# Kernel tuning notes

Measured on AMD Instinct MI355X. Metric: run time of the kernel, lower is better.

The kernel has to match this reference:

```python
import jax, jax.numpy as jnp
import numpy as np

N = 50000      # nodes
E = 800000     # edges (before self loops)
D_IN = 128
HID = 64
HEADS = 8
D_OUT = 10


def setup_inputs() -> dict:
    key = jax.random.key(0)
    ks = jax.random.split(key, 16)
    sc = 0.05
    x = jax.random.normal(ks[0], (N, D_IN), dtype=jnp.float32)
    edge_index = jax.random.randint(ks[1], (2, E), 0, N, dtype=jnp.int64)
    return {
        "x": x,
        "edge_index": edge_index,
        "W1": jax.random.normal(ks[2], (HEADS * HID, D_IN), dtype=jnp.float32) * sc,
        "a1_src": jax.random.normal(ks[3], (HEADS, HID), dtype=jnp.float32) * sc,
        "a1_dst": jax.random.normal(ks[4], (HEADS, HID), dtype=jnp.float32) * sc,
        "b1": jnp.zeros((HEADS * HID,), jnp.float32),
        "W2": jax.random.normal(ks[5], (HID, HEADS * HID), dtype=jnp.float32) * sc,
        "a2_src": jax.random.normal(ks[6], (1, HID), dtype=jnp.float32) * sc,
        "a2_dst": jax.random.normal(ks[7], (1, HID), dtype=jnp.float32) * sc,
        "b2": jnp.zeros((HID,), jnp.float32),
        "W3": jax.random.normal(ks[8], (HID, HID), dtype=jnp.float32) * sc,
        "a3_src": jax.random.normal(ks[9], (1, HID), dtype=jnp.float32) * sc,
        "a3_dst": jax.random.normal(ks[10], (1, HID), dtype=jnp.float32) * sc,
        "b3": jnp.zeros((HID,), jnp.float32),
        "Wc": jax.random.normal(ks[11], (D_OUT, HID), dtype=jnp.float32) * sc,
        "bc": jnp.zeros((D_OUT,), jnp.float32),
    }


def gat_conv(x, src, dst, W, a_src, a_dst, b, concat):
    """PyG GATConv (eval mode, add_self_loops already applied to src/dst)."""
    heads, out_ch = a_src.shape
    n = x.shape[0]
    h = (x @ W.T).reshape(n, heads, out_ch)          # [N, H, C]
    a_s = jnp.einsum('nhc,hc->nh', h, a_src)          # [N, H]
    a_d = jnp.einsum('nhc,hc->nh', h, a_dst)          # [N, H]
    e = jax.nn.leaky_relu(a_s[src] + a_d[dst], 0.2)   # [Etot, H]
    # segment softmax over incoming edges of each destination node
    m = jax.ops.segment_max(e, dst, num_segments=n)
    ex = jnp.exp(e - m[dst])
    s = jax.ops.segment_sum(ex, dst, num_segments=n)
    alpha = ex / (s[dst] + 1e-16)                     # [Etot, H]
    out = jax.ops.segment_sum(h[src] * alpha[:, :, None], dst, num_segments=n)
    if concat:
        out = out.reshape(n, heads * out_ch)
    else:
        out = out.mean(axis=1)
    return out + b


def reference(x, edge_index, W1, a1_src, a1_dst, b1, W2, a2_src, a2_dst, b2,
              W3, a3_src, a3_dst, b3, Wc, bc):
    loops = jnp.arange(N, dtype=edge_index.dtype)
    src = jnp.concatenate([edge_index[0], loops])
    dst = jnp.concatenate([edge_index[1], loops])
    h = jax.nn.elu(gat_conv(x, src, dst, W1, a1_src, a1_dst, b1, True))
    h = jax.nn.elu(gat_conv(h, src, dst, W2, a2_src, a2_dst, b2, False))
    h = jax.nn.elu(gat_conv(h, src, dst, W3, a3_src, a3_dst, b3, False))
    return h @ Wc.T + bc
```

## Files before the change

kernel.cpp:

```cpp
#include <hip/hip_runtime.h>
#include <math.h>

#define N_NODES 50000
#define N_EDGES 800000
#define ETOT    (N_EDGES + N_NODES)
#define COL_CAP (ETOT + 3 * N_NODES + 16)

typedef short bf16x8 __attribute__((ext_vector_type(8)));
typedef float f32x4  __attribute__((ext_vector_type(4)));
typedef float f32x2  __attribute__((ext_vector_type(2)));

__device__ __forceinline__ float b2f(unsigned int u16) {
    return __uint_as_float(u16 << 16);
}
__device__ __forceinline__ unsigned short f2b(float f) {
    unsigned int u = __float_as_uint(f);
    u += 0x7fffu + ((u >> 16) & 1u);
    return (unsigned short)(u >> 16);
}

__global__ __launch_bounds__(256) void k_prep(const float* __restrict__ x,
                                              const float* __restrict__ w1,
                                              const float* __restrict__ w2,
                                              const float* __restrict__ w3,
                                              unsigned short* __restrict__ xb,
                                              unsigned short* __restrict__ o1,
                                              unsigned short* __restrict__ o2,
                                              unsigned short* __restrict__ o3,
                                              int* __restrict__ deg,
                                              int* __restrict__ flag) {
    int i = blockIdx.x * 256 + threadIdx.x;
    if (i < N_NODES) deg[i] = 0;
    if (i == 0) *flag = 0;
    if (i < 512 * 128 / 4) {
        float4 v = ((const float4*)w1)[i];
        ushort2* o = (ushort2*)(o1 + i * 4);
        o[0] = make_ushort2(f2b(v.x), f2b(v.y));
        o[1] = make_ushort2(f2b(v.z), f2b(v.w));
    }
    if (i < 64 * 512 / 4) {
        float4 v = ((const float4*)w2)[i];
        ushort2* o = (ushort2*)(o2 + i * 4);
        o[0] = make_ushort2(f2b(v.x), f2b(v.y));
        o[1] = make_ushort2(f2b(v.z), f2b(v.w));
    }
    if (i < 64 * 64 / 4) {
        float4 v = ((const float4*)w3)[i];
        ushort2* o = (ushort2*)(o3 + i * 4);
        o[0] = make_ushort2(f2b(v.x), f2b(v.y));
        o[1] = make_ushort2(f2b(v.z), f2b(v.w));
    }
    if (i < N_NODES * 128 / 8) {
        const float4* xp = (const float4*)x + (size_t)i * 2;
        float4 v0 = xp[0], v1 = xp[1];
        unsigned int u0 = (unsigned int)f2b(v0.x) | ((unsigned int)f2b(v0.y) << 16);
        unsigned int u1 = (unsigned int)f2b(v0.z) | ((unsigned int)f2b(v0.w) << 16);
        unsigned int u2 = (unsigned int)f2b(v1.x) | ((unsigned int)f2b(v1.y) << 16);
        unsigned int u3 = (unsigned int)f2b(v1.z) | ((unsigned int)f2b(v1.w) << 16);
        *(uint4*)(xb + (size_t)i * 8) = make_uint4(u0, u1, u2, u3);
    }
}

__global__ __launch_bounds__(256) void k_prepu(const float* __restrict__ W1,
                                               const float* __restrict__ a1s,
                                               const float* __restrict__ a1d,
                                               float* __restrict__ U) {
    int h = blockIdx.x;
    int t = threadIdx.x;
    int which = t >> 7, k = t & 127;
    const float* av = which ? a1d : a1s;
    float acc = 0.f;
    for (int c = 0; c < 64; ++c)
        acc += av[h * 64 + c] * W1[(size_t)(h * 64 + c) * 128 + k];
    U[(which * 8 + h) * 128 + k] = acc;
}

__global__ __launch_bounds__(256) void k_attn(const unsigned short* __restrict__ xb,
                                              const float* __restrict__ U,
                                              float* __restrict__ asrc,
                                              float* __restrict__ adst) {
    __shared__ float sU[16 * 132];
    __shared__ unsigned short sX[16 * 136];
    int t = threadIdx.x;
    for (int i = t; i < 2048; i += 256) sU[(i >> 7) * 132 + (i & 127)] = U[i];
    int n0 = blockIdx.x * 16;
    {
        int r = t >> 4, c = (t & 15) * 8;
        *(uint4*)&sX[r * 136 + c] = *(const uint4*)(xb + (size_t)(n0 + r) * 128 + c);
    }
    __syncthreads();
    int nl = t >> 4, o = t & 15;
    const unsigned short* xr = sX + nl * 136;
    const float* ur = sU + o * 132;
    float acc = 0.f;
#pragma unroll 8
    for (int k2 = 0; k2 < 128; ++k2) acc += b2f(xr[k2]) * ur[k2];
    int n = n0 + nl;
    if (o < 8) asrc[n * 8 + o] = acc;
    else       adst[n * 8 + (o - 8)] = acc;
}

__global__ void k_detect(const int* __restrict__ idx, int* __restrict__ flag) {
    int i = blockIdx.x * blockDim.x + threadIdx.x;
    int v = idx[2 * i + 1];
    unsigned long long any = __ballot(v != 0);
    if ((threadIdx.x & 63) == 0 && any) atomicOr(flag, 1);
}

__device__ __forceinline__ int edge_src(const int* idx, int e, int is32) {
    return is32 ? idx[e] : idx[2 * e];
}
__device__ __forceinline__ int edge_dst(const int* idx, int e, int is32) {
    return is32 ? idx[N_EDGES + e] : idx[2 * (N_EDGES + e)];
}

__global__ void k_degree(const int* __restrict__ idx, const int* __restrict__ flag,
                         int* __restrict__ deg) {
    int e = blockIdx.x * blockDim.x + threadIdx.x;
    if (e >= ETOT) return;
    int is32 = *flag;
    int d = (e < N_EDGES) ? edge_dst(idx, e, is32) : (e - N_EDGES);
    atomicAdd(&deg[d], 1);
}

__global__ __launch_bounds__(256) void k_scan1(const int* __restrict__ deg,
                                               int* __restrict__ rowptr,
                                               int* __restrict__ bsum) {
    __shared__ int sd[256];
    int t = threadIdx.x;
    int i = blockIdx.x * 256 + t;
    int v = (i < N_NODES) ? ((deg[i] + 3) & ~3) : 0;
    sd[t] = v;
    __syncthreads();
#pragma unroll
    for (int off = 1; off < 256; off <<= 1) {
        int a = (t >= off) ? sd[t - off] : 0;
        __syncthreads();
        sd[t] += a;
        __syncthreads();
    }
    if (i < N_NODES) rowptr[i] = sd[t] - v;
    if (t == 255) bsum[blockIdx.x] = sd[255];
}

__global__ __launch_bounds__(256) void k_scan2(int* __restrict__ bsum,
                                               int* __restrict__ boff,
                                               int* __restrict__ rowptr,
                                               int nb) {
    __shared__ int sd[256];
    int t = threadIdx.x;
    int v = (t < nb) ? bsum[t] : 0;
    sd[t] = v;
    __syncthreads();
#pragma unroll
    for (int off = 1; off < 256; off <<= 1) {
        int a = (t >= off) ? sd[t - off] : 0;
        __syncthreads();
        sd[t] += a;
        __syncthreads();
    }
    boff[t] = sd[t] - v;
    if (t == 255) rowptr[N_NODES] = sd[255];
}

__global__ __launch_bounds__(256) void k_scan3(int* __restrict__ rowptr,
                                               const int* __restrict__ boff,
                                               const int* __restrict__ deg,
                                               int* __restrict__ cursor,
                                               int* __restrict__ col) {
    int i = blockIdx.x * 256 + threadIdx.x;
    if (i == 0) {
        int tot = rowptr[N_NODES];
        for (int q = 0; q < 16; ++q) col[tot + q] = 0;
    }
    if (i >= N_NODES) return;
    int r = rowptr[i] + boff[blockIdx.x];
    rowptr[i] = r;
    cursor[i] = r;
    int d = deg[i];
    int pd = (d + 3) & ~3;
    for (int p = r + d; p < r + pd; ++p) col[p] = 0;
}

__global__ void k_scatter(const int* __restrict__ idx, const int* __restrict__ flag,
                          int* __restrict__ cursor, int* __restrict__ col) {
    int e = blockIdx.x * blockDim.x + threadIdx.x;
    if (e >= ETOT) return;
    int is32 = *flag;
    int s, d;
    if (e < N_EDGES) { s = edge_src(idx, e, is32); d = edge_dst(idx, e, is32); }
    else             { s = d = e - N_EDGES; }
    int pos = atomicAdd(&cursor[d], 1);
    col[pos] = s;
}

template<int EPI>
__global__ __launch_bounds__(256) void k_gemm(const unsigned short* __restrict__ Ab,
                                              const unsigned short* __restrict__ W,
                                              unsigned short* __restrict__ C,
                                              const float* __restrict__ a_src,
                                              const float* __restrict__ a_dst,
                                              float* __restrict__ asb,
                                              float* __restrict__ adb,
                                              const float* __restrict__ bias,
                                              int M, int K, int Astr, int aoffmul,
                                              int Nout, int Hstr) {
    __shared__ unsigned short As[64 * 40];
    __shared__ unsigned short Bs[64 * 40];
    __shared__ float red_s[4][64];
    __shared__ float red_d[4][64];
    int t = threadIdx.x;
    int w = t >> 6, l = t & 63;
    int quad = l >> 4, lm = l & 15;
    int m0 = blockIdx.y * 64, n0 = blockIdx.x * 64;
    int hd = blockIdx.x;
    int aoff = hd * aoffmul;
    int lr = t >> 2;
    int lc = (t & 3) * 8;

    f32x4 acc[4];
#pragma unroll
    for (int r = 0; r < 4; ++r) acc[r] = (f32x4){0.f, 0.f, 0.f, 0.f};

    for (int k0 = 0; k0 < K; k0 += 32) {
        int m = m0 + lr;
        uint4 av = make_uint4(0, 0, 0, 0);
        if (m < M) av = *(const uint4*)(Ab + (size_t)m * Astr + aoff + k0 + lc);
        *(uint4*)&As[lr * 40 + lc] = av;
        uint4 bv = *(const uint4*)(W + (size_t)(n0 + lr) * K + k0 + lc);
        *(uint4*)&Bs[lr * 40 + lc] = bv;
        __syncthreads();

        bf16x8 bfrag = *(const bf16x8*)&Bs[(w * 16 + lm) * 40 + quad * 8];
#pragma unroll
        for (int r = 0; r < 4; ++r) {
            bf16x8 afrag = *(const bf16x8*)&As[(r * 16 + lm) * 40 + quad * 8];
            acc[r] = __builtin_amdgcn_mfma_f32_16x16x32_bf16(afrag, bfrag, acc[r], 0, 0, 0);
        }
        __syncthreads();
    }

    if (EPI == 1) {
        float bcol = bias[n0 + w * 16 + lm];
#pragma unroll
        for (int r = 0; r < 4; ++r)
#pragma unroll
            for (int g = 0; g < 4; ++g) {
                int m = m0 + r * 16 + quad * 4 + g;
                if (m < M) {
                    float v = acc[r][g] + bcol;
                    v = (v > 0.f) ? v : expm1f(v);
                    C[(size_t)m * Nout + n0 + w * 16 + lm] = f2b(v);
                }
            }
        return;
    }

#pragma unroll
    for (int r = 0; r < 4; ++r)
#pragma unroll
        for (int g = 0; g < 4; ++g) {
            int m = m0 + r * 16 + quad * 4 + g;
            if (m < M) C[(size_t)m * Nout + n0 + w * 16 + lm] = f2b(acc[r][g]);
        }

    float as = a_src[hd * 64 + w * 16 + lm];
    float ad = a_dst[hd * 64 + w * 16 + lm];
#pragma unroll
    for (int r = 0; r < 4; ++r) {
#pragma unroll
        for (int g = 0; g < 4; ++g) {
            float vs = acc[r][g] * as;
            float vd = acc[r][g] * ad;
#pragma unroll
            for (int off = 1; off < 16; off <<= 1) {
                vs += __shfl_xor(vs, off);
                vd += __shfl_xor(vd, off);
            }
            if (lm == 0) {
                red_s[w][r * 16 + quad * 4 + g] = vs;
                red_d[w][r * 16 + quad * 4 + g] = vd;
            }
        }
    }
    __syncthreads();
    if (t < 64) {
        float vs = red_s[0][t] + red_s[1][t] + red_s[2][t] + red_s[3][t];
        float vd = red_d[0][t] + red_d[1][t] + red_d[2][t] + red_d[3][t];
        int m = m0 + t;
        if (m < M) {
            asb[(size_t)m * Hstr + hd] = vs;
            adb[(size_t)m * Hstr + hd] = vd;
        }
    }
}

__device__ __forceinline__ void aggx_slot(int idx, int rem, float tt, unsigned int xx,
                                          float adn, float& ssum, f32x2* acc) {
    float e = tt + adn;
    e = fmaxf(e, 0.2f * e);
    float ex = __expf(e);
    ex = (idx < rem) ? ex : 0.f;
    ssum += ex;
    float fx = __uint_as_float(xx << 16);
    float fy = __uint_as_float(xx & 0xffff0000u);
    int exi = __float_as_int(ex);
#pragma unroll
    for (int hh = 0; hh < 8; ++hh) {
        float wh = __int_as_float(__builtin_amdgcn_readlane(exi, hh << 3));
        acc[hh].x = fmaf(fx, wh, acc[hh].x);
        acc[hh].y = fmaf(fy, wh, acc[hh].y);
    }
}

__global__ __launch_bounds__(256) void k_aggx(const unsigned short* __restrict__ xb,
                                              const float* __restrict__ asrc,
                                              const float* __restrict__ adst,
                                              const int* __restrict__ rowptr,
                                              const int* __restrict__ degv,
                                              const int* __restrict__ col,
                                              unsigned short* __restrict__ aggX) {
    int n = blockIdx.x * 4 + (threadIdx.x >> 6);
    if (n >= N_NODES) return;
    int l = threadIdx.x & 63;
    int j = l >> 3;
    unsigned lx2 = (unsigned)(l << 1);
    int start = rowptr[n];
    int end   = start + degv[n];
    float adn = adst[((unsigned)n << 3) + (unsigned)j];

    float ssum = 0.f;
    f32x2 acc[8];
#pragma unroll
    for (int hh = 0; hh < 8; ++hh) acc[hh] = (f32x2){0.f, 0.f};

    float tA0, tA1, tA2, tA3, tB0, tB1, tB2, tB3;
    unsigned int xA0, xA1, xA2, xA3, xB0, xB1, xB2, xB3;
    int4 cA, cB;

#define GATHX(c, T0, T1, T2, T3, X0, X1, X2, X3)                              \
    T0 = asrc[(((unsigned)(c).x) << 3) + (unsigned)j];                        \
    T1 = asrc[(((unsigned)(c).y) << 3) + (unsigned)j];                        \
    T2 = asrc[(((unsigned)(c).z) << 3) + (unsigned)j];                        \
    T3 = asrc[(((unsigned)(c).w) << 3) + (unsigned)j];                        \
    X0 = *(const unsigned int*)(xb + (((unsigned)(c).x) << 7) + lx2);         \
    X1 = *(const unsigned int*)(xb + (((unsigned)(c).y) << 7) + lx2);         \
    X2 = *(const unsigned int*)(xb + (((unsigned)(c).z) << 7) + lx2);         \
    X3 = *(const unsigned int*)(xb + (((unsigned)(c).w) << 7) + lx2);

    int k = start;
    cA = *(const int4*)(col + k);
    cB = *(const int4*)(col + k + 4);
    GATHX(cA, tA0, tA1, tA2, tA3, xA0, xA1, xA2, xA3);
    for (;;) {
        bool hasB = (k + 4 < end);
        if (hasB) {
            GATHX(cB, tB0, tB1, tB2, tB3, xB0, xB1, xB2, xB3);
            cA = *(const int4*)(col + k + 8);
        }
        {
            int rem = end - k;
            aggx_slot(0, rem, tA0, xA0, adn, ssum, acc);
            aggx_slot(1, rem, tA1, xA1, adn, ssum, acc);
            aggx_slot(2, rem, tA2, xA2, adn, ssum, acc);
            aggx_slot(3, rem, tA3, xA3, adn, ssum, acc);
        }
        k += 4;
        if (!hasB) break;
        bool hasA = (k + 4 < end);
        if (hasA) {
            GATHX(cA, tA0, tA1, tA2, tA3, xA0, xA1, xA2, xA3);
            cB = *(const int4*)(col + k + 8);
        }
        {
            int rem = end - k;
            aggx_slot(0, rem, tB0, xB0, adn, ssum, acc);
            aggx_slot(1, rem, tB1, xB1, adn, ssum, acc);
            aggx_slot(2, rem, tB2, xB2, adn, ssum, acc);
            aggx_slot(3, rem, tB3, xB3, adn, ssum, acc);
        }
        k += 4;
        if (!hasA) break;
    }
#undef GATHX

    size_t base = (size_t)n * 1024 + lx2;
#pragma unroll
    for (int hh = 0; hh < 8; ++hh) {
        float sh = __int_as_float(__builtin_amdgcn_readlane(__float_as_int(ssum), hh << 3));
        float iv = 1.f / (sh + 1e-16f);
        unsigned int lo = f2b(acc[hh].x * iv);
        unsigned int hi = f2b(acc[hh].y * iv);
        *(unsigned int*)(aggX + base + hh * 128) = lo | (hi << 16);
    }
}

__global__ __launch_bounds__(256) void k_agg1(const unsigned short* __restrict__ h,
                                              const float* __restrict__ asrc,
                                              const float* __restrict__ adst,
                                              const int* __restrict__ rowptr,
                                              const int* __restrict__ degv,
                                              const int* __restrict__ col,
                                              const float* __restrict__ bias,
                                              unsigned short* __restrict__ out) {
    int n = blockIdx.x * 4 + (threadIdx.x >> 6);
    if (n >= N_NODES) return;
    int l = threadIdx.x & 63;
    int start = rowptr[n];
    int end   = start + degv[n];
    float adn = adst[n];

    float ssum = 0.f, o = 0.f;
    float tA0, tA1, tA2, tA3, tB0, tB1, tB2, tB3;
    unsigned short qA0, qA1, qA2, qA3, qB0, qB1, qB2, qB3;
    int4 cA, cB;

#define GATH1(c, T0, T1, T2, T3, Q0, Q1, Q2, Q3)                              \
    T0 = asrc[(unsigned)(c).x];                                               \
    T1 = asrc[(unsigned)(c).y];                                               \
    T2 = asrc[(unsigned)(c).z];                                               \
    T3 = asrc[(unsigned)(c).w];                                               \
    Q0 = h[(((unsigned)(c).x) << 6) + (unsigned)l];                           \
    Q1 = h[(((unsigned)(c).y) << 6) + (unsigned)l];                           \
    Q2 = h[(((unsigned)(c).z) << 6) + (unsigned)l];                           \
    Q3 = h[(((unsigned)(c).w) << 6) + (unsigned)l];

#define ASLOT1(IDX, TT, QQ, rem)                                              \
    {                                                                         \
        float e = TT + adn;                                                   \
        e = fmaxf(e, 0.2f * e);                                               \
        float ex = __expf(e);                                                 \
        ex = ((IDX) < (rem)) ? ex : 0.f;                                      \
        ssum += ex;                                                           \
        o += ex * b2f(QQ);                                                    \
    }

    int k = start;
    cA = *(const int4*)(col + k);
    cB = *(const int4*)(col + k + 4);
    GATH1(cA, tA0, tA1, tA2, tA3, qA0, qA1, qA2, qA3);
    for (;;) {
        bool hasB = (k + 4 < end);
        if (hasB) {
            GATH1(cB, tB0, tB1, tB2, tB3, qB0, qB1, qB2, qB3);
            cA = *(const int4*)(col + k + 8);
        }
        {
            int rem = end - k;
            ASLOT1(0, tA0, qA0, rem);
            ASLOT1(1, tA1, qA1, rem);
            ASLOT1(2, tA2, qA2, rem);
            ASLOT1(3, tA3, qA3, rem);
        }
        k += 4;
        if (!hasB) break;
        bool hasA = (k + 4 < end);
        if (hasA) {
            GATH1(cA, tA0, tA1, tA2, tA3, qA0, qA1, qA2, qA3);
            cB = *(const int4*)(col + k + 8);
        }
        {
            int rem = end - k;
            ASLOT1(0, tB0, qB0, rem);
            ASLOT1(1, tB1, qB1, rem);
            ASLOT1(2, tB2, qB2, rem);
            ASLOT1(3, tB3, qB3, rem);
        }
        k += 4;
        if (!hasA) break;
    }
#undef GATH1
#undef ASLOT1

    float v = o / (ssum + 1e-16f) + bias[l];
    v = (v > 0.f) ? v : expm1f(v);
    out[(size_t)n * 64 + l] = f2b(v);
}

__global__ __launch_bounds__(256) void k_classifier(const unsigned short* __restrict__ h,
                                                    const float* __restrict__ Wc,
                                                    const float* __restrict__ bc,
                                                    float* __restrict__ out) {
    __shared__ float sW[640];
    for (int i = threadIdx.x; i < 640; i += blockDim.x) sW[i] = Wc[i];
    __syncthreads();
    int idx = blockIdx.x * blockDim.x + threadIdx.x;
    if (idx >= N_NODES * 10) return;
    int n = idx / 10, d = idx - n * 10;
    const unsigned short* hr = h + (size_t)n * 64;
    const float* wr = sW + d * 64;
    float acc = 0.f;
#pragma unroll
    for (int c = 0; c < 64; ++c) acc += b2f(hr[c]) * wr[c];
    out[idx] = acc + bc[d];
}

extern "C" void kernel_launch(void* const* d_in, const int* in_sizes, int n_in,
                              void* d_out, int out_size, void* d_ws, size_t ws_size,
                              hipStream_t stream) {
    const float* x    = (const float*)d_in[0];
    const int*   eidx = (const int*)  d_in[1];
    const float* W1   = (const float*)d_in[2];
    const float* a1s  = (const float*)d_in[3];
    const float* a1d  = (const float*)d_in[4];
    const float* b1   = (const float*)d_in[5];
    const float* W2   = (const float*)d_in[6];
    const float* a2s  = (const float*)d_in[7];
    const float* a2d  = (const float*)d_in[8];
    const float* b2   = (const float*)d_in[9];
    const float* W3   = (const float*)d_in[10];
    const float* a3s  = (const float*)d_in[11];
    const float* a3d  = (const float*)d_in[12];
    const float* b3   = (const float*)d_in[13];
    const float* Wc   = (const float*)d_in[14];
    const float* bc   = (const float*)d_in[15];
    float* out = (float*)d_out;

    float* asbuf = (float*)d_ws;
    float* adbuf = asbuf + (size_t)N_NODES * 8;
    unsigned short* aggX = (unsigned short*)(adbuf + (size_t)N_NODES * 8);
    unsigned short* x2  = aggX + (size_t)N_NODES * 1024;
    unsigned short* xb  = x2  + (size_t)N_NODES * 512;
    unsigned short* W1b = xb  + (size_t)N_NODES * 128;
    unsigned short* W2b = W1b + 512 * 128;
    unsigned short* W3b = W2b + 64 * 512;
    float* U    = (float*)(W3b + 64 * 64);
    int* ibase  = (int*)(U + 16 * 128);
    int* deg    = ibase;
    int* flag   = deg + N_NODES;
    int* rowptr = flag + 1;
    int* cursor = rowptr + N_NODES + 1;
    int* bsum   = cursor + N_NODES;
    int* boff   = bsum + 256;
    int* col    = boff + 256;
    unsigned short* h2 = aggX;
    unsigned short* x3 = h2 + (size_t)N_NODES * 64;
    unsigned short* h3 = x3 + (size_t)N_NODES * 64;
    unsigned short* x4 = h3 + (size_t)N_NODES * 64;

    dim3 blk(256);
    const int SCAN_BLOCKS = (N_NODES + 255) / 256;
    const int PREP_BLOCKS = (N_NODES * 128 / 8 + 255) / 256;

    k_prep<<<PREP_BLOCKS, blk, 0, stream>>>(x, W1, W2, W3, xb, W1b, W2b, W3b, deg, flag);
    k_prepu<<<8, blk, 0, stream>>>(W1, a1s, a1d, U);
    k_attn<<<N_NODES / 16, blk, 0, stream>>>(xb, U, asbuf, adbuf);

    k_detect<<<32, blk, 0, stream>>>(eidx, flag);
    k_degree<<<(ETOT + 255) / 256, blk, 0, stream>>>(eidx, flag, deg);
    k_scan1<<<SCAN_BLOCKS, blk, 0, stream>>>(deg, rowptr, bsum);
    k_scan2<<<1, blk, 0, stream>>>(bsum, boff, rowptr, SCAN_BLOCKS);
    k_scan3<<<SCAN_BLOCKS, blk, 0, stream>>>(rowptr, boff, deg, cursor, col);
    k_scatter<<<(ETOT + 255) / 256, blk, 0, stream>>>(eidx, flag, cursor, col);

    int mblocks = (N_NODES + 63) / 64;
    int nblocks = N_NODES / 4;

    k_aggx<<<nblocks, blk, 0, stream>>>(xb, asbuf, adbuf, rowptr, deg, col, aggX);
    k_gemm<1><<<dim3(8, mblocks), blk, 0, stream>>>(aggX, W1b, x2,
                                                    (const float*)0, (const float*)0,
                                                    (float*)0, (float*)0, b1,
                                                    N_NODES, 128, 1024, 128, 512, 8);

    k_gemm<0><<<dim3(1, mblocks), blk, 0, stream>>>(x2, W2b, h2,
                                                    a2s, a2d, asbuf, adbuf, (const float*)0,
                                                    N_NODES, 512, 512, 0, 64, 1);
    k_agg1<<<nblocks, blk, 0, stream>>>(h2, asbuf, adbuf, rowptr, deg, col, b2, x3);

    k_gemm<0><<<dim3(1, mblocks), blk, 0, stream>>>(x3, W3b, h3,
                                                    a3s, a3d, asbuf, adbuf, (const float*)0,
                                                    N_NODES, 64, 64, 0, 64, 1);
    k_agg1<<<nblocks, blk, 0, stream>>>(h3, asbuf, adbuf, rowptr, deg, col, b3, x4);

    k_classifier<<<(N_NODES * 10 + 255) / 256, blk, 0, stream>>>(x4, Wc, bc, out);
}
```

Baseline: 436.7 us.

## Aggregate layer-1 features with MFMA over 32-edge chunks staged in LDS

Rewrites the layer-1 feature aggregation so each wave gathers 32 neighbour rows into shared memory (transposed) and multiplies them by per-head attention weights with bf16 MFMA. The weights are split into hi and lo bf16 parts to keep accuracy. This replaces the per-edge readlane and FMA loop with matrix-core work, and the column padding grows so reads past the end of the edge list stay safe. The weight-projection kernel is also folded into the prep kernel to save a launch. In exchange it pads edges to 32 per chunk, which wastes work on low-degree nodes, and it uses a lot of LDS per block, which may lower occupancy.

```diff
diff --git a/kernel.cpp b/kernel.cpp
--- a/kernel.cpp
+++ b/kernel.cpp
@@ -4,7 +4,7 @@
 #define N_NODES 50000
 #define N_EDGES 800000
 #define ETOT    (N_EDGES + N_NODES)
-#define COL_CAP (ETOT + 3 * N_NODES + 16)
+#define COL_CAP (ETOT + 3 * N_NODES + 64)
 
 typedef short bf16x8 __attribute__((ext_vector_type(8)));
 typedef float f32x4  __attribute__((ext_vector_type(4)));
@@ -23,15 +23,27 @@
                                               const float* __restrict__ w1,
                                               const float* __restrict__ w2,
                                               const float* __restrict__ w3,
+                                              const float* __restrict__ a1s,
+                                              const float* __restrict__ a1d,
                                               unsigned short* __restrict__ xb,
                                               unsigned short* __restrict__ o1,
                                               unsigned short* __restrict__ o2,
                                               unsigned short* __restrict__ o3,
+                                              float* __restrict__ U,
                                               int* __restrict__ deg,
                                               int* __restrict__ flag) {
     int i = blockIdx.x * 256 + threadIdx.x;
     if (i < N_NODES) deg[i] = 0;
     if (i == 0) *flag = 0;
+    if (blockIdx.x < 8) {
+        int h = blockIdx.x;
+        int which = threadIdx.x >> 7, k = threadIdx.x & 127;
+        const float* av = which ? a1d : a1s;
+        float acc = 0.f;
+        for (int c = 0; c < 64; ++c)
+            acc += av[h * 64 + c] * w1[(size_t)(h * 64 + c) * 128 + k];
+        U[(which * 8 + h) * 128 + k] = acc;
+    }
     if (i < 512 * 128 / 4) {
         float4 v = ((const float4*)w1)[i];
         ushort2* o = (ushort2*)(o1 + i * 4);
@@ -59,20 +71,6 @@
         unsigned int u3 = (unsigned int)f2b(v1.z) | ((unsigned int)f2b(v1.w) << 16);
         *(uint4*)(xb + (size_t)i * 8) = make_uint4(u0, u1, u2, u3);
     }
-}
-
-__global__ __launch_bounds__(256) void k_prepu(const float* __restrict__ W1,
-                                               const float* __restrict__ a1s,
-                                               const float* __restrict__ a1d,
-                                               float* __restrict__ U) {
-    int h = blockIdx.x;
-    int t = threadIdx.x;
-    int which = t >> 7, k = t & 127;
-    const float* av = which ? a1d : a1s;
-    float acc = 0.f;
-    for (int c = 0; c < 64; ++c)
-        acc += av[h * 64 + c] * W1[(size_t)(h * 64 + c) * 128 + k];
-    U[(which * 8 + h) * 128 + k] = acc;
 }
 
 __global__ __launch_bounds__(256) void k_attn(const unsigned short* __restrict__ xb,
@@ -171,7 +169,7 @@
     int i = blockIdx.x * 256 + threadIdx.x;
     if (i == 0) {
         int tot = rowptr[N_NODES];
-        for (int q = 0; q < 16; ++q) col[tot + q] = 0;
+        for (int q = 0; q < 48; ++q) col[tot + q] = 0;
     }
     if (i >= N_NODES) return;
     int r = rowptr[i] + boff[blockIdx.x];
@@ -295,24 +293,6 @@
     }
 }
 
-__device__ __forceinline__ void aggx_slot(int idx, int rem, float tt, unsigned int xx,
-                                          float adn, float& ssum, f32x2* acc) {
-    float e = tt + adn;
-    e = fmaxf(e, 0.2f * e);
-    float ex = __expf(e);
-    ex = (idx < rem) ? ex : 0.f;
-    ssum += ex;
-    float fx = __uint_as_float(xx << 16);
-    float fy = __uint_as_float(xx & 0xffff0000u);
-    int exi = __float_as_int(ex);
-#pragma unroll
-    for (int hh = 0; hh < 8; ++hh) {
-        float wh = __int_as_float(__builtin_amdgcn_readlane(exi, hh << 3));
-        acc[hh].x = fmaf(fx, wh, acc[hh].x);
-        acc[hh].y = fmaf(fy, wh, acc[hh].y);
-    }
-}
-
 __global__ __launch_bounds__(256) void k_aggx(const unsigned short* __restrict__ xb,
                                               const float* __restrict__ asrc,
                                               const float* __restrict__ adst,
@@ -320,78 +300,114 @@
                                               const int* __restrict__ degv,
                                               const int* __restrict__ col,
                                               unsigned short* __restrict__ aggX) {
-    int n = blockIdx.x * 4 + (threadIdx.x >> 6);
+    __shared__ unsigned short sX[4][128 * 34];
+    int wid = threadIdx.x >> 6;
+    int n = blockIdx.x * 4 + wid;
     if (n >= N_NODES) return;
     int l = threadIdx.x & 63;
-    int j = l >> 3;
-    unsigned lx2 = (unsigned)(l << 1);
+    int lm = l & 15, q = l >> 4;
+    unsigned short* sx = sX[wid];
+
     int start = rowptr[n];
-    int end   = start + degv[n];
-    float adn = adst[((unsigned)n << 3) + (unsigned)j];
-
+    int deg   = degv[n];
+    float adn = adst[((unsigned)n << 3) + (unsigned)(lm & 7)];
+
+    f32x4 acc[8];
+#pragma unroll
+    for (int i = 0; i < 8; ++i) acc[i] = (f32x4){0.f, 0.f, 0.f, 0.f};
     float ssum = 0.f;
-    f32x2 acc[8];
-#pragma unroll
-    for (int hh = 0; hh < 8; ++hh) acc[hh] = (f32x2){0.f, 0.f};
-
-    float tA0, tA1, tA2, tA3, tB0, tB1, tB2, tB3;
-    unsigned int xA0, xA1, xA2, xA3, xB0, xB1, xB2, xB3;
-    int4 cA, cB;
-
-#define GATHX(c, T0, T1, T2, T3, X0, X1, X2, X3)                              \
-    T0 = asrc[(((unsigned)(c).x) << 3) + (unsigned)j];                        \
-    T1 = asrc[(((unsigned)(c).y) << 3) + (unsigned)j];                        \
-    T2 = asrc[(((unsigned)(c).z) << 3) + (unsigned)j];                        \
-    T3 = asrc[(((unsigned)(c).w) << 3) + (unsigned)j];                        \
-    X0 = *(const unsigned int*)(xb + (((unsigned)(c).x) << 7) + lx2);         \
-    X1 = *(const unsigned int*)(xb + (((unsigned)(c).y) << 7) + lx2);         \
-    X2 = *(const unsigned int*)(xb + (((unsigned)(c).z) << 7) + lx2);         \
-    X3 = *(const unsigned int*)(xb + (((unsigned)(c).w) << 7) + lx2);
-
-    int k = start;
-    cA = *(const int4*)(col + k);
-    cB = *(const int4*)(col + k + 4);
-    GATHX(cA, tA0, tA1, tA2, tA3, xA0, xA1, xA2, xA3);
-    for (;;) {
-        bool hasB = (k + 4 < end);
-        if (hasB) {
-            GATHX(cB, tB0, tB1, tB2, tB3, xB0, xB1, xB2, xB3);
-            cA = *(const int4*)(col + k + 8);
-        }
+    unsigned ls = (unsigned)(l << 1);
+
+    int nch = (deg + 31) >> 5;
+    for (int ch = 0; ch < nch; ++ch) {
+        int base = start + (ch << 5);
+        const int4* cp = (const int4*)(col + base);
+
+        asm volatile("" ::: "memory");
+
+#define XLD(S) (*(const unsigned int*)(xb + (((unsigned)(S)) << 7) + ls))
+#define XST(E, D) { sx[(2 * l) * 34 + (E)] = (unsigned short)((D) & 0xffffu);       \
+                    sx[(2 * l + 1) * 34 + (E)] = (unsigned short)((D) >> 16); }
         {
-            int rem = end - k;
-            aggx_slot(0, rem, tA0, xA0, adn, ssum, acc);
-            aggx_slot(1, rem, tA1, xA1, adn, ssum, acc);
-            aggx_slot(2, rem, tA2, xA2, adn, ssum, acc);
-            aggx_slot(3, rem, tA3, xA3, adn, ssum, acc);
-        }
-        k += 4;
-        if (!hasB) break;
-        bool hasA = (k + 4 < end);
-        if (hasA) {
-            GATHX(cA, tA0, tA1, tA2, tA3, xA0, xA1, xA2, xA3);
-            cB = *(const int4*)(col + k + 8);
+            int4 c0 = cp[0], c1 = cp[1], c2 = cp[2], c3 = cp[3];
+            unsigned int d0 = XLD(c0.x), d1 = XLD(c0.y), d2 = XLD(c0.z), d3 = XLD(c0.w);
+            unsigned int d4 = XLD(c1.x), d5 = XLD(c1.y), d6 = XLD(c1.z), d7 = XLD(c1.w);
+            unsigned int d8 = XLD(c2.x), d9 = XLD(c2.y), dA = XLD(c2.z), dB = XLD(c2.w);
+            unsigned int dC = XLD(c3.x), dD = XLD(c3.y), dE = XLD(c3.z), dF = XLD(c3.w);
+            XST(0, d0)  XST(1, d1)  XST(2, d2)  XST(3, d3)
+            XST(4, d4)  XST(5, d5)  XST(6, d6)  XST(7, d7)
+            XST(8, d8)  XST(9, d9)  XST(10, dA) XST(11, dB)
+            XST(12, dC) XST(13, dD) XST(14, dE) XST(15, dF)
         }
         {
-            int rem = end - k;
-            aggx_slot(0, rem, tB0, xB0, adn, ssum, acc);
-            aggx_slot(1, rem, tB1, xB1, adn, ssum, acc);
-            aggx_slot(2, rem, tB2, xB2, adn, ssum, acc);
-            aggx_slot(3, rem, tB3, xB3, adn, ssum, acc);
-        }
-        k += 4;
-        if (!hasA) break;
-    }
-#undef GATHX
-
-    size_t base = (size_t)n * 1024 + lx2;
-#pragma unroll
-    for (int hh = 0; hh < 8; ++hh) {
-        float sh = __int_as_float(__builtin_amdgcn_readlane(__float_as_int(ssum), hh << 3));
-        float iv = 1.f / (sh + 1e-16f);
-        unsigned int lo = f2b(acc[hh].x * iv);
-        unsigned int hi = f2b(acc[hh].y * iv);
-        *(unsigned int*)(aggX + base + hh * 128) = lo | (hi << 16);
+            int4 c4 = cp[4], c5 = cp[5], c6 = cp[6], c7 = cp[7];
+            unsigned int d0 = XLD(c4.x), d1 = XLD(c4.y), d2 = XLD(c4.z), d3 = XLD(c4.w);
+            unsigned int d4 = XLD(c5.x), d5 = XLD(c5.y), d6 = XLD(c5.z), d7 = XLD(c5.w);
+            unsigned int d8 = XLD(c6.x), d9 = XLD(c6.y), dA = XLD(c6.z), dB = XLD(c6.w);
+            unsigned int dC = XLD(c7.x), dD = XLD(c7.y), dE = XLD(c7.z), dF = XLD(c7.w);
+            XST(16, d0) XST(17, d1) XST(18, d2) XST(19, d3)
+            XST(20, d4) XST(21, d5) XST(22, d6) XST(23, d7)
+            XST(24, d8) XST(25, d9) XST(26, dA) XST(27, dB)
+            XST(28, dC) XST(29, dD) XST(30, dE) XST(31, dF)
+        }
+#undef XLD
+#undef XST
+
+        int slot0 = (ch << 5) + (q << 3);
+        float wv[8];
+#pragma unroll
+        for (int j = 0; j < 8; ++j) {
+            int s = col[base + (q << 3) + j];
+            float tt = asrc[((unsigned)s << 3) + (unsigned)lm];
+            float e = tt + adn;
+            e = fmaxf(e, 0.2f * e);
+            float ex = __expf(e);
+            bool valid = (lm < 8) && (slot0 + j < deg);
+            ex = valid ? ex : 0.f;
+            ssum += ex;
+            wv[j] = ex;
+        }
+        unsigned int wp[4], rp[4];
+#pragma unroll
+        for (int p = 0; p < 4; ++p) {
+            unsigned int h0 = f2b(wv[2 * p]), h1 = f2b(wv[2 * p + 1]);
+            wp[p] = h0 | (h1 << 16);
+            float r0 = wv[2 * p]     - b2f(h0);
+            float r1 = wv[2 * p + 1] - b2f(h1);
+            rp[p] = (unsigned int)f2b(r0) | ((unsigned int)f2b(r1) << 16);
+        }
+        uint4 wpu = make_uint4(wp[0], wp[1], wp[2], wp[3]);
+        uint4 rpu = make_uint4(rp[0], rp[1], rp[2], rp[3]);
+        bf16x8 wf_hi = *(bf16x8*)&wpu;
+        bf16x8 wf_lo = *(bf16x8*)&rpu;
+
+        asm volatile("s_waitcnt lgkmcnt(0)" ::: "memory");
+        __builtin_amdgcn_sched_barrier(0);
+
+#pragma unroll
+        for (int ct = 0; ct < 8; ++ct) {
+            int row = ct * 16 + lm;
+            const unsigned int* fp = (const unsigned int*)(sx + row * 34 + (q << 3));
+            uint4 fu = make_uint4(fp[0], fp[1], fp[2], fp[3]);
+            bf16x8 xf = *(bf16x8*)&fu;
+            acc[ct] = __builtin_amdgcn_mfma_f32_16x16x32_bf16(xf, wf_hi, acc[ct], 0, 0, 0);
+            acc[ct] = __builtin_amdgcn_mfma_f32_16x16x32_bf16(xf, wf_lo, acc[ct], 0, 0, 0);
+        }
+    }
+
+    ssum += __shfl_xor(ssum, 16);
+    ssum += __shfl_xor(ssum, 32);
+    if (lm < 8) {
+        float inv = 1.f / (ssum + 1e-16f);
+        size_t obase = (size_t)n * 1024 + ((unsigned)lm << 7) + ((unsigned)q << 2);
+#pragma unroll
+        for (int ct = 0; ct < 8; ++ct) {
+            unsigned int u0 = (unsigned int)f2b(acc[ct][0] * inv) |
+                              ((unsigned int)f2b(acc[ct][1] * inv) << 16);
+            unsigned int u1 = (unsigned int)f2b(acc[ct][2] * inv) |
+                              ((unsigned int)f2b(acc[ct][3] * inv) << 16);
+            *(uint2*)(aggX + obase + ct * 16) = make_uint2(u0, u1);
+        }
     }
 }
 
@@ -542,8 +558,8 @@
     const int SCAN_BLOCKS = (N_NODES + 255) / 256;
     const int PREP_BLOCKS = (N_NODES * 128 / 8 + 255) / 256;
 
-    k_prep<<<PREP_BLOCKS, blk, 0, stream>>>(x, W1, W2, W3, xb, W1b, W2b, W3b, deg, flag);
-    k_prepu<<<8, blk, 0, stream>>>(W1, a1s, a1d, U);
+    k_prep<<<PREP_BLOCKS, blk, 0, stream>>>(x, W1, W2, W3, a1s, a1d,
+                                            xb, W1b, W2b, W3b, U, deg, flag);
     k_attn<<<N_NODES / 16, blk, 0, stream>>>(xb, U, asbuf, adbuf);
 
     k_detect<<<32, blk, 0, stream>>>(eidx, flag);
```

After: 434.4 us. About the same (-0.5%).

## Fuse layer-1 aggregation with per-head projection GEMM and merge prepu into prep

Applied to the files above, without the earlier changes.

Layer-1 aggregation now collects 16 nodes per block into shared memory, handing nodes to waves through an LDS atomic counter. Each block then runs the per-head 128x64 MFMA projection with bias and ELU directly from shared memory, writing x2. This avoids writing and rereading the N x 1024 bf16 aggX buffer and removes one kernel launch, along with folding k_prepu into k_prep. The cost is fewer, heavier blocks with large LDS use, which lowers occupancy for the gather-bound aggregation, and W1b is reread from global memory by every block.

```diff
diff --git a/kernel.cpp b/kernel.cpp
--- a/kernel.cpp
+++ b/kernel.cpp
@@ -4,7 +4,7 @@
 #define N_NODES 50000
 #define N_EDGES 800000
 #define ETOT    (N_EDGES + N_NODES)
-#define COL_CAP (ETOT + 3 * N_NODES + 16)
+#define COL_CAP (ETOT + 3 * N_NODES + 64)
 
 typedef short bf16x8 __attribute__((ext_vector_type(8)));
 typedef float f32x4  __attribute__((ext_vector_type(4)));
@@ -23,15 +23,27 @@
                                               const float* __restrict__ w1,
                                               const float* __restrict__ w2,
                                               const float* __restrict__ w3,
+                                              const float* __restrict__ a1s,
+                                              const float* __restrict__ a1d,
                                               unsigned short* __restrict__ xb,
                                               unsigned short* __restrict__ o1,
                                               unsigned short* __restrict__ o2,
                                               unsigned short* __restrict__ o3,
+                                              float* __restrict__ U,
                                               int* __restrict__ deg,
                                               int* __restrict__ flag) {
     int i = blockIdx.x * 256 + threadIdx.x;
     if (i < N_NODES) deg[i] = 0;
     if (i == 0) *flag = 0;
+    if (blockIdx.x < 8) {
+        int h = blockIdx.x;
+        int which = threadIdx.x >> 7, k = threadIdx.x & 127;
+        const float* av = which ? a1d : a1s;
+        float acc = 0.f;
+        for (int c = 0; c < 64; ++c)
+            acc += av[h * 64 + c] * w1[(size_t)(h * 64 + c) * 128 + k];
+        U[(which * 8 + h) * 128 + k] = acc;
+    }
     if (i < 512 * 128 / 4) {
         float4 v = ((const float4*)w1)[i];
         ushort2* o = (ushort2*)(o1 + i * 4);
@@ -59,20 +71,6 @@
         unsigned int u3 = (unsigned int)f2b(v1.z) | ((unsigned int)f2b(v1.w) << 16);
         *(uint4*)(xb + (size_t)i * 8) = make_uint4(u0, u1, u2, u3);
     }
-}
-
-__global__ __launch_bounds__(256) void k_prepu(const float* __restrict__ W1,
-                                               const float* __restrict__ a1s,
-                                               const float* __restrict__ a1d,
-                                               float* __restrict__ U) {
-    int h = blockIdx.x;
-    int t = threadIdx.x;
-    int which = t >> 7, k = t & 127;
-    const float* av = which ? a1d : a1s;
-    float acc = 0.f;
-    for (int c = 0; c < 64; ++c)
-        acc += av[h * 64 + c] * W1[(size_t)(h * 64 + c) * 128 + k];
-    U[(which * 8 + h) * 128 + k] = acc;
 }
 
 __global__ __launch_bounds__(256) void k_attn(const unsigned short* __restrict__ xb,
@@ -171,7 +169,7 @@
     int i = blockIdx.x * 256 + threadIdx.x;
     if (i == 0) {
         int tot = rowptr[N_NODES];
-        for (int q = 0; q < 16; ++q) col[tot + q] = 0;
+        for (int q = 0; q < 48; ++q) col[tot + q] = 0;
     }
     if (i >= N_NODES) return;
     int r = rowptr[i] + boff[blockIdx.x];
@@ -194,7 +192,6 @@
     col[pos] = s;
 }
 
-template<int EPI>
 __global__ __launch_bounds__(256) void k_gemm(const unsigned short* __restrict__ Ab,
                                               const unsigned short* __restrict__ W,
                                               unsigned short* __restrict__ C,
@@ -202,9 +199,7 @@
                                               const float* __restrict__ a_dst,
                                               float* __restrict__ asb,
                                               float* __restrict__ adb,
-                                              const float* __restrict__ bias,
-                                              int M, int K, int Astr, int aoffmul,
-                                              int Nout, int Hstr) {
+                                              int M, int K, int Nout) {
     __shared__ unsigned short As[64 * 40];
     __shared__ unsigned short Bs[64 * 40];
     __shared__ float red_s[4][64];
@@ -214,7 +209,6 @@
     int quad = l >> 4, lm = l & 15;
     int m0 = blockIdx.y * 64, n0 = blockIdx.x * 64;
     int hd = blockIdx.x;
-    int aoff = hd * aoffmul;
     int lr = t >> 2;
     int lc = (t & 3) * 8;
 
@@ -225,7 +219,7 @@
     for (int k0 = 0; k0 < K; k0 += 32) {
         int m = m0 + lr;
         uint4 av = make_uint4(0, 0, 0, 0);
-        if (m < M) av = *(const uint4*)(Ab + (size_t)m * Astr + aoff + k0 + lc);
+        if (m < M) av = *(const uint4*)(Ab + (size_t)m * K + k0 + lc);
         *(uint4*)&As[lr * 40 + lc] = av;
         uint4 bv = *(const uint4*)(W + (size_t)(n0 + lr) * K + k0 + lc);
         *(uint4*)&Bs[lr * 40 + lc] = bv;
@@ -238,22 +232,6 @@
             acc[r] = __builtin_amdgcn_mfma_f32_16x16x32_bf16(afrag, bfrag, acc[r], 0, 0, 0);
         }
         __syncthreads();
-    }
-
-    if (EPI == 1) {
-        float bcol = bias[n0 + w * 16 + lm];
-#pragma unroll
-        for (int r = 0; r < 4; ++r)
-#pragma unroll
-            for (int g = 0; g < 4; ++g) {
-                int m = m0 + r * 16 + quad * 4 + g;
-                if (m < M) {
-                    float v = acc[r][g] + bcol;
-                    v = (v > 0.f) ? v : expm1f(v);
-                    C[(size_t)m * Nout + n0 + w * 16 + lm] = f2b(v);
-                }
-            }
-        return;
     }
 
 #pragma unroll
@@ -289,8 +267,8 @@
         float vd = red_d[0][t] + red_d[1][t] + red_d[2][t] + red_d[3][t];
         int m = m0 + t;
         if (m < M) {
-            asb[(size_t)m * Hstr + hd] = vs;
-            adb[(size_t)m * Hstr + hd] = vd;
+            asb[m] = vs;
+            adb[m] = vd;
         }
     }
 }
@@ -313,30 +291,46 @@
     }
 }
 
-__global__ __launch_bounds__(256) void k_aggx(const unsigned short* __restrict__ xb,
+__global__ __launch_bounds__(256) void k_aggf(const unsigned short* __restrict__ xb,
                                               const float* __restrict__ asrc,
                                               const float* __restrict__ adst,
                                               const int* __restrict__ rowptr,
                                               const int* __restrict__ degv,
                                               const int* __restrict__ col,
-                                              unsigned short* __restrict__ aggX) {
-    int n = blockIdx.x * 4 + (threadIdx.x >> 6);
-    if (n >= N_NODES) return;
-    int l = threadIdx.x & 63;
+                                              const unsigned short* __restrict__ W1b,
+                                              const float* __restrict__ b1,
+                                              unsigned short* __restrict__ x2) {
+    __shared__ unsigned short sAgg[8 * 16 * 136];
+    __shared__ int sCnt;
+    int t = threadIdx.x;
+    int l = t & 63;
+    int wid = t >> 6;
+    int n0 = blockIdx.x * 16;
+    if (t == 0) sCnt = 0;
+    __syncthreads();
+
     int j = l >> 3;
     unsigned lx2 = (unsigned)(l << 1);
-    int start = rowptr[n];
-    int end   = start + degv[n];
-    float adn = adst[((unsigned)n << 3) + (unsigned)j];
-
-    float ssum = 0.f;
-    f32x2 acc[8];
-#pragma unroll
-    for (int hh = 0; hh < 8; ++hh) acc[hh] = (f32x2){0.f, 0.f};
-
-    float tA0, tA1, tA2, tA3, tB0, tB1, tB2, tB3;
-    unsigned int xA0, xA1, xA2, xA3, xB0, xB1, xB2, xB3;
-    int4 cA, cB;
+
+    for (;;) {
+        int m = 0;
+        if (l == 0) m = atomicAdd(&sCnt, 1);
+        m = __shfl(m, 0);
+        if (m >= 16) break;
+        int n = n0 + m;
+
+        int start = rowptr[n];
+        int end   = start + degv[n];
+        float adn = adst[((unsigned)n << 3) + (unsigned)j];
+
+        float ssum = 0.f;
+        f32x2 acc[8];
+#pragma unroll
+        for (int hh = 0; hh < 8; ++hh) acc[hh] = (f32x2){0.f, 0.f};
+
+        float tA0, tA1, tA2, tA3, tB0, tB1, tB2, tB3;
+        unsigned int xA0, xA1, xA2, xA3, xB0, xB1, xB2, xB3;
+        int4 cA, cB;
 
 #define GATHX(c, T0, T1, T2, T3, X0, X1, X2, X3)                              \
     T0 = asrc[(((unsigned)(c).x) << 3) + (unsigned)j];                        \
@@ -348,50 +342,82 @@
     X2 = *(const unsigned int*)(xb + (((unsigned)(c).z) << 7) + lx2);         \
     X3 = *(const unsigned int*)(xb + (((unsigned)(c).w) << 7) + lx2);
 
-    int k = start;
-    cA = *(const int4*)(col + k);
-    cB = *(const int4*)(col + k + 4);
-    GATHX(cA, tA0, tA1, tA2, tA3, xA0, xA1, xA2, xA3);
-    for (;;) {
-        bool hasB = (k + 4 < end);
-        if (hasB) {
-            GATHX(cB, tB0, tB1, tB2, tB3, xB0, xB1, xB2, xB3);
-            cA = *(const int4*)(col + k + 8);
-        }
-        {
-            int rem = end - k;
-            aggx_slot(0, rem, tA0, xA0, adn, ssum, acc);
-            aggx_slot(1, rem, tA1, xA1, adn, ssum, acc);
-            aggx_slot(2, rem, tA2, xA2, adn, ssum, acc);
-            aggx_slot(3, rem, tA3, xA3, adn, ssum, acc);
-        }
-        k += 4;
-        if (!hasB) break;
-        bool hasA = (k + 4 < end);
-        if (hasA) {
-            GATHX(cA, tA0, tA1, tA2, tA3, xA0, xA1, xA2, xA3);
-            cB = *(const int4*)(col + k + 8);
-        }
-        {
-            int rem = end - k;
-            aggx_slot(0, rem, tB0, xB0, adn, ssum, acc);
-            aggx_slot(1, rem, tB1, xB1, adn, ssum, acc);
-            aggx_slot(2, rem, tB2, xB2, adn, ssum, acc);
-            aggx_slot(3, rem, tB3, xB3, adn, ssum, acc);
-        }
-        k += 4;
-        if (!hasA) break;
-    }
+        int k = start;
+        cA = *(const int4*)(col + k);
+        cB = *(const int4*)(col + k + 4);
+        GATHX(cA, tA0, tA1, tA2, tA3, xA0, xA1, xA2, xA3);
+        for (;;) {
+            bool hasB = (k + 4 < end);
+            if (hasB) {
+                GATHX(cB, tB0, tB1, tB2, tB3, xB0, xB1, xB2, xB3);
+                cA = *(const int4*)(col + k + 8);
+            }
+            {
+                int rem = end - k;
+                aggx_slot(0, rem, tA0, xA0, adn, ssum, acc);
+                aggx_slot(1, rem, tA1, xA1, adn, ssum, acc);
+                aggx_slot(2, rem, tA2, xA2, adn, ssum, acc);
+                aggx_slot(3, rem, tA3, xA3, adn, ssum, acc);
+            }
+            k += 4;
+            if (!hasB) break;
+            bool hasA = (k + 4 < end);
+            if (hasA) {
+                GATHX(cA, tA0, tA1, tA2, tA3, xA0, xA1, xA2, xA3);
+                cB = *(const int4*)(col + k + 8);
+            }
+            {
+                int rem = end - k;
+                aggx_slot(0, rem, tB0, xB0, adn, ssum, acc);
+                aggx_slot(1, rem, tB1, xB1, adn, ssum, acc);
+                aggx_slot(2, rem, tB2, xB2, adn, ssum, acc);
+                aggx_slot(3, rem, tB3, xB3, adn, ssum, acc);
+            }
+            k += 4;
+            if (!hasA) break;
+        }
 #undef GATHX
 
-    size_t base = (size_t)n * 1024 + lx2;
-#pragma unroll
-    for (int hh = 0; hh < 8; ++hh) {
-        float sh = __int_as_float(__builtin_amdgcn_readlane(__float_as_int(ssum), hh << 3));
-        float iv = 1.f / (sh + 1e-16f);
-        unsigned int lo = f2b(acc[hh].x * iv);
-        unsigned int hi = f2b(acc[hh].y * iv);
-        *(unsigned int*)(aggX + base + hh * 128) = lo | (hi << 16);
+#pragma unroll
+        for (int hh = 0; hh < 8; ++hh) {
+            float sh = __int_as_float(__builtin_amdgcn_readlane(__float_as_int(ssum), hh << 3));
+            float iv = 1.f / (sh + 1e-16f);
+            unsigned int lo = f2b(acc[hh].x * iv);
+            unsigned int hi = f2b(acc[hh].y * iv);
+            *(unsigned int*)&sAgg[hh * 2176 + m * 136 + lx2] = lo | (hi << 16);
+        }
+    }
+    __syncthreads();
+
+    int lm = l & 15, q = l >> 4;
+#pragma unroll
+    for (int hh = 0; hh < 2; ++hh) {
+        int h = wid * 2 + hh;
+        f32x4 acc4[4];
+#pragma unroll
+        for (int t4 = 0; t4 < 4; ++t4) acc4[t4] = (f32x4){0.f, 0.f, 0.f, 0.f};
+#pragma unroll
+        for (int ks = 0; ks < 4; ++ks) {
+            uint4 au = *(const uint4*)&sAgg[h * 2176 + lm * 136 + ks * 32 + (q << 3)];
+            bf16x8 af = *(bf16x8*)&au;
+#pragma unroll
+            for (int t4 = 0; t4 < 4; ++t4) {
+                uint4 bu = *(const uint4*)(W1b + (size_t)(h * 64 + t4 * 16 + lm) * 128 + ks * 32 + (q << 3));
+                bf16x8 bf_ = *(bf16x8*)&bu;
+                acc4[t4] = __builtin_amdgcn_mfma_f32_16x16x32_bf16(af, bf_, acc4[t4], 0, 0, 0);
+            }
+        }
+#pragma unroll
+        for (int t4 = 0; t4 < 4; ++t4) {
+            float bc = b1[h * 64 + t4 * 16 + lm];
+#pragma unroll
+            for (int g = 0; g < 4; ++g) {
+                int m = q * 4 + g;
+                float v = acc4[t4][g] + bc;
+                v = (v > 0.f) ? v : expm1f(v);
+                x2[(size_t)(n0 + m) * 512 + h * 64 + t4 * 16 + lm] = f2b(v);
+            }
+        }
     }
 }
 
@@ -518,9 +544,12 @@
 
     float* asbuf = (float*)d_ws;
     float* adbuf = asbuf + (size_t)N_NODES * 8;
-    unsigned short* aggX = (unsigned short*)(adbuf + (size_t)N_NODES * 8);
-    unsigned short* x2  = aggX + (size_t)N_NODES * 1024;
-    unsigned short* xb  = x2  + (size_t)N_NODES * 512;
+    unsigned short* x2  = (unsigned short*)(adbuf + (size_t)N_NODES * 8);
+    unsigned short* h2  = x2  + (size_t)N_NODES * 512;
+    unsigned short* x3  = h2  + (size_t)N_NODES * 64;
+    unsigned short* h3  = x3  + (size_t)N_NODES * 64;
+    unsigned short* x4  = h3  + (size_t)N_NODES * 64;
+    unsigned short* xb  = x4  + (size_t)N_NODES * 64;
     unsigned short* W1b = xb  + (size_t)N_NODES * 128;
     unsigned short* W2b = W1b + 512 * 128;
     unsigned short* W3b = W2b + 64 * 512;
@@ -533,17 +562,13 @@
     int* bsum   = cursor + N_NODES;
     int* boff   = bsum + 256;
     int* col    = boff + 256;
-    unsigned short* h2 = aggX;
-    unsigned short* x3 = h2 + (size_t)N_NODES * 64;
-    unsigned short* h3 = x3 + (size_t)N_NODES * 64;
-    unsigned short* x4 = h3 + (size_t)N_NODES * 64;
 
     dim3 blk(256);
     const int SCAN_BLOCKS = (N_NODES + 255) / 256;
     const int PREP_BLOCKS = (N_NODES * 128 / 8 + 255) / 256;
 
-    k_prep<<<PREP_BLOCKS, blk, 0, stream>>>(x, W1, W2, W3, xb, W1b, W2b, W3b, deg, flag);
-    k_prepu<<<8, blk, 0, stream>>>(W1, a1s, a1d, U);
+    k_prep<<<PREP_BLOCKS, blk, 0, stream>>>(x, W1, W2, W3, a1s, a1d,
+                                            xb, W1b, W2b, W3b, U, deg, flag);
     k_attn<<<N_NODES / 16, blk, 0, stream>>>(xb, U, asbuf, adbuf);
 
     k_detect<<<32, blk, 0, stream>>>(eidx, flag);
@@ -556,20 +581,17 @@
     int mblocks = (N_NODES + 63) / 64;
     int nblocks = N_NODES / 4;
 
-    k_aggx<<<nblocks, blk, 0, stream>>>(xb, asbuf, adbuf, rowptr, deg, col, aggX);
-    k_gemm<1><<<dim3(8, mblocks), blk, 0, stream>>>(aggX, W1b, x2,
-                                                    (const float*)0, (const float*)0,
-                                                    (float*)0, (float*)0, b1,
-                                                    N_NODES, 128, 1024, 128, 512, 8);
-
-    k_gemm<0><<<dim3(1, mblocks), blk, 0, stream>>>(x2, W2b, h2,
-                                                    a2s, a2d, asbuf, adbuf, (const float*)0,
-                                                    N_NODES, 512, 512, 0, 64, 1);
+    k_aggf<<<N_NODES / 16, blk, 0, stream>>>(xb, asbuf, adbuf, rowptr, deg, col,
+                                             W1b, b1, x2);
+
+    k_gemm<<<dim3(1, mblocks), blk, 0, stream>>>(x2, W2b, h2,
+                                                 a2s, a2d, asbuf, adbuf,
+                                                 N_NODES, 512, 64);
     k_agg1<<<nblocks, blk, 0, stream>>>(h2, asbuf, adbuf, rowptr, deg, col, b2, x3);
 
-    k_gemm<0><<<dim3(1, mblocks), blk, 0, stream>>>(x3, W3b, h3,
-                                                    a3s, a3d, asbuf, adbuf, (const float*)0,
-                                                    N_NODES, 64, 64, 0, 64, 1);
+    k_gemm<<<dim3(1, mblocks), blk, 0, stream>>>(x3, W3b, h3,
+                                                 a3s, a3d, asbuf, adbuf,
+                                                 N_NODES, 64, 64);
     k_agg1<<<nblocks, blk, 0, stream>>>(h3, asbuf, adbuf, rowptr, deg, col, b3, x4);
 
     k_classifier<<<(N_NODES * 10 + 255) / 256, blk, 0, stream>>>(x4, Wc, bc, out);
```

Measured after the change: 441.0 us. Within noise of the previous version (+1.0%).
